# Kernel tuning notes

Measured on AMD Instinct MI355X. Metric: run time of the kernel, lower is better.

## Reference

```python
import jax, jax.numpy as jnp
import numpy as np

B, T, D, H, L, V = 16, 1024, 512, 8, 6, 96
HS = D // H
FF = 4 * D


def setup_inputs() -> dict:
    key = jax.random.key(0)
    ks = jax.random.split(key, 16)
    n = lambda k, shape: jax.random.normal(k, shape, jnp.float32) * 0.02
    return {
        "idx": jax.random.randint(ks[0], (B, T), 0, V),
        "targets": jax.random.randint(ks[1], (B, T), 0, V),
        "tok_emb": n(ks[2], (V, D)),
        "pos_emb": n(ks[3], (T, D)),
        "Wq": n(ks[4], (L, H, D, HS)),
        "Wk": n(ks[5], (L, H, D, HS)),
        "Wv": n(ks[6], (L, H, D, HS)),
        "Wproj": n(ks[7], (L, D, D)),
        "bproj": jnp.zeros((L, D), jnp.float32),
        "W1": n(ks[8], (L, D, FF)),
        "b1": jnp.zeros((L, FF), jnp.float32),
        "W2": n(ks[9], (L, FF, D)),
        "b2": jnp.zeros((L, D), jnp.float32),
        "ln1_s": jnp.ones((L, D), jnp.float32),
        "ln1_b": jnp.zeros((L, D), jnp.float32),
        "ln2_s": jnp.ones((L, D), jnp.float32),
        "ln2_b": jnp.zeros((L, D), jnp.float32),
        "lnf_s": jnp.ones((D,), jnp.float32),
        "lnf_b": jnp.zeros((D,), jnp.float32),
        "Wout": n(ks[10], (D, V)),
        "bout": jnp.zeros((V,), jnp.float32),
    }


def _ln(x, s, b, eps=1e-5):
    m = x.mean(-1, keepdims=True)
    v = ((x - m) ** 2).mean(-1, keepdims=True)
    return (x - m) * jax.lax.rsqrt(v + eps) * s + b


def reference(idx, targets, tok_emb, pos_emb, Wq, Wk, Wv, Wproj, bproj,
              W1, b1, W2, b2, ln1_s, ln1_b, ln2_s, ln2_b, lnf_s, lnf_b,
              Wout, bout):
    x = tok_emb[idx] + pos_emb[:T]  # [B,T,D]
    causal = jnp.tril(jnp.ones((T, T), jnp.bool_))
    scale = D ** (-0.5)  # NOTE: source scales by full channel dim, not head_size
    for l in range(L):
        h = _ln(x, ln1_s[l], ln1_b[l])
        q = jnp.einsum("btd,hdk->bhtk", h, Wq[l])
        k = jnp.einsum("btd,hdk->bhtk", h, Wk[l])
        v = jnp.einsum("btd,hdk->bhtk", h, Wv[l])
        att = jnp.einsum("bhtk,bhsk->bhts", q, k) * scale
        att = jnp.where(causal, att, -jnp.inf)
        att = jax.nn.softmax(att, axis=-1)
        o = jnp.einsum("bhts,bhsk->bhtk", att, v)
        o = o.transpose(0, 2, 1, 3).reshape(B, T, D)  # concat heads
        x = x + (o @ Wproj[l] + bproj[l])
        h2 = _ln(x, ln2_s[l], ln2_b[l])
        x = x + (jnp.maximum(h2 @ W1[l] + b1[l], 0.0) @ W2[l] + b2[l])
    x = _ln(x, lnf_s, lnf_b)
    logits = (x @ Wout + bout).reshape(B * T, V)
    logp = jax.nn.log_softmax(logits, axis=-1)
    loss = -logp[jnp.arange(B * T), targets.reshape(-1)].mean()
    return logits, loss
```

## Files before the change

kernel.cpp:

```cpp
#include <hip/hip_runtime.h>

#define B_  16
#define T_  1024
#define D_  512
#define H_  8
#define L_  6
#define V_  96
#define HS_ 64
#define FF_ 2048
#define BT_ (B_*T_)
#define QKS 1024

typedef __attribute__((ext_vector_type(8))) short bf16x8;
typedef __attribute__((ext_vector_type(4))) float f32x4;

typedef __attribute__((address_space(3))) unsigned int lds_u32_t;
typedef const __attribute__((address_space(1))) unsigned int glb_u32_t;

__device__ __forceinline__ void gload16(const unsigned short* g, unsigned short* l) {
  __builtin_amdgcn_global_load_lds((glb_u32_t*)g, (lds_u32_t*)l, 16, 0, 0);
}

__device__ __forceinline__ unsigned short f2b(float f) {
  unsigned u = __float_as_uint(f);
  unsigned r = (u + 0x7FFFu + ((u >> 16) & 1u)) >> 16;
  return (unsigned short)r;
}

__global__ void zero_kernel(float* p) { p[0] = 0.f; }

__global__ __launch_bounds__(128) void embed_kernel(const int* __restrict__ idx,
    const float* __restrict__ tok, const float* __restrict__ pos, float* __restrict__ x) {
  int bt = blockIdx.x;
  int t  = bt & (T_ - 1);
  int id = idx[bt];
  if (id < 0) id = 0; if (id > V_ - 1) id = V_ - 1;
  int d  = threadIdx.x * 4;
  float4 tv = *(const float4*)(tok + (size_t)id * D_ + d);
  float4 pv = *(const float4*)(pos + (size_t)t  * D_ + d);
  float4 o = {tv.x + pv.x, tv.y + pv.y, tv.z + pv.z, tv.w + pv.w};
  *(float4*)(x + (size_t)bt * D_ + d) = o;
}

__global__ __launch_bounds__(256) void transpose_cvt(const float* __restrict__ src,
    unsigned short* __restrict__ dst, int R, int C, long sstride, long dstride,
    int zper, long zouter) {
  __shared__ float t[32][33];
  const float* s = src + (size_t)blockIdx.z * sstride;
  unsigned short* d = dst + (size_t)(blockIdx.z / zper) * zouter
                          + (size_t)(blockIdx.z % zper) * dstride;
  int r0 = blockIdx.y * 32, c0 = blockIdx.x * 32;
  int tr = threadIdx.x >> 5, tc = threadIdx.x & 31;
#pragma unroll
  for (int i = 0; i < 4; ++i)
    t[tr + i * 8][tc] = s[(size_t)(r0 + tr + i * 8) * C + c0 + tc];
  __syncthreads();
#pragma unroll
  for (int i = 0; i < 4; ++i)
    d[(size_t)(c0 + tr + i * 8) * R + r0 + tc] = f2b(t[tc][tr + i * 8]);
}

template<bool BF16OUT>
__global__ __launch_bounds__(256) void ln_kernel(const float* __restrict__ x,
    const float* __restrict__ s, const float* __restrict__ b, void* __restrict__ outv) {
  int wave = threadIdx.x >> 6;
  int lane = threadIdx.x & 63;
  int r = blockIdx.x * 4 + wave;
  const float* xr = x + (size_t)r * D_ + lane * 8;
  float4 va = *(const float4*)(xr);
  float4 vb = *(const float4*)(xr + 4);
  float vals[8] = {va.x, va.y, va.z, va.w, vb.x, vb.y, vb.z, vb.w};
  float sum = 0.f;
#pragma unroll
  for (int j = 0; j < 8; ++j) sum += vals[j];
#pragma unroll
  for (int o = 32; o > 0; o >>= 1) sum += __shfl_xor(sum, o, 64);
  float mean = sum * (1.f / D_);
  float vs = 0.f;
#pragma unroll
  for (int j = 0; j < 8; ++j) { float d = vals[j] - mean; vs += d * d; }
#pragma unroll
  for (int o = 32; o > 0; o >>= 1) vs += __shfl_xor(vs, o, 64);
  float rstd = rsqrtf(vs * (1.f / D_) + 1e-5f);
  float4 sa = *(const float4*)(s + lane * 8);
  float4 sb = *(const float4*)(s + lane * 8 + 4);
  float4 ba = *(const float4*)(b + lane * 8);
  float4 bb = *(const float4*)(b + lane * 8 + 4);
  float sc[8] = {sa.x, sa.y, sa.z, sa.w, sb.x, sb.y, sb.z, sb.w};
  float bc[8] = {ba.x, ba.y, ba.z, ba.w, bb.x, bb.y, bb.z, bb.w};
  float v[8];
#pragma unroll
  for (int j = 0; j < 8; ++j) v[j] = (vals[j] - mean) * rstd * sc[j] + bc[j];
  if (BF16OUT) {
    uint4 pk;
    pk.x = (unsigned)f2b(v[0]) | ((unsigned)f2b(v[1]) << 16);
    pk.y = (unsigned)f2b(v[2]) | ((unsigned)f2b(v[3]) << 16);
    pk.z = (unsigned)f2b(v[4]) | ((unsigned)f2b(v[5]) << 16);
    pk.w = (unsigned)f2b(v[6]) | ((unsigned)f2b(v[7]) << 16);
    *(uint4*)((unsigned short*)outv + (size_t)r * D_ + lane * 8) = pk;
  } else {
    float* op = (float*)outv + (size_t)r * D_ + lane * 8;
    *(float4*)(op)     = make_float4(v[0], v[1], v[2], v[3]);
    *(float4*)(op + 4) = make_float4(v[4], v[5], v[6], v[7]);
  }
}

#define BK 32
template<bool ACC, bool RELU, bool BIAS, int OUTMODE, int MT, int NT>
__global__ __launch_bounds__(256) void mfma_gemm(
    const unsigned short* __restrict__ A,
    const unsigned short* __restrict__ Bt,
    const float* __restrict__ bias,
    void* __restrict__ Cv, void* __restrict__ Cv2,
    int K, int ldc) {
  constexpr int NI = (MT == 128) ? 4 : (NT == 128 ? 2 : 1);
  constexpr int WN = (MT == 128) ? 64 : (NT == 128 ? 32 : 16);
  __shared__ unsigned short Al[2][MT * BK];
  __shared__ unsigned short Bl[2][NT * BK];
  const int nwg = gridDim.x * gridDim.y;
  const int flat = blockIdx.x + gridDim.x * blockIdx.y;
  const int swz = (flat & 7) * (nwg >> 3) + (flat >> 3);
  const int bx = swz / gridDim.y;
  const int by = swz % gridDim.y;
  const int m0 = bx * MT, n0 = by * NT;
  const int tid = threadIdx.x;
  const int lane = tid & 63, wave = tid >> 6;
  const int wy = (MT == 128) ? (wave >> 1) : 0;
  const int wx = (MT == 128) ? (wave & 1) : wave;
  const int l15 = lane & 15, quad = lane >> 4;

  const int sbase = wave * 1024;
  const int soff  = sbase + lane * 16;
  const int r0 = soff >> 6, c0e = (soff & 63) >> 1;
  const int r1 = r0 + 64;
  const int ls = sbase >> 1;
  const unsigned short* gA0 = A  + (size_t)(m0 + r0) * K + c0e;
  const unsigned short* gA1 = A  + (size_t)(m0 + r1) * K + c0e;
  const unsigned short* gB0 = Bt + (size_t)(n0 + r0) * K + c0e;
  const unsigned short* gB1 = Bt + (size_t)(n0 + r1) * K + c0e;

  auto stage = [&](int buf, int k0) {
    gload16(gA0 + k0, &Al[buf][ls]);
    if constexpr (MT == 128) gload16(gA1 + k0, &Al[buf][ls + 2048]);
    gload16(gB0 + k0, &Bl[buf][ls]);
    if constexpr (NT == 128) gload16(gB1 + k0, &Bl[buf][ls + 2048]);
  };

  f32x4 acc[4][NI];
  const f32x4 z4 = {0.f, 0.f, 0.f, 0.f};
#pragma unroll
  for (int mi = 0; mi < 4; ++mi)
#pragma unroll
    for (int ni = 0; ni < NI; ++ni) acc[mi][ni] = z4;

  stage(0, 0);
  __syncthreads();

  const int nsteps = K / BK;
  int cur = 0;
  for (int s = 0; s < nsteps; ++s) {
    if (s + 1 < nsteps) stage(cur ^ 1, (s + 1) * BK);
    bf16x8 af[4], bfr[NI];
#pragma unroll
    for (int mi = 0; mi < 4; ++mi)
      af[mi] = *(const bf16x8*)(&Al[cur][(wy * 64 + mi * 16 + l15) * BK + quad * 8]);
#pragma unroll
    for (int ni = 0; ni < NI; ++ni)
      bfr[ni] = *(const bf16x8*)(&Bl[cur][(wx * WN + ni * 16 + l15) * BK + quad * 8]);
#pragma unroll
    for (int mi = 0; mi < 4; ++mi)
#pragma unroll
      for (int ni = 0; ni < NI; ++ni)
        acc[mi][ni] = __builtin_amdgcn_mfma_f32_16x16x32_bf16(af[mi], bfr[ni], acc[mi][ni], 0, 0, 0);
    if (s + 1 < nsteps) {
      __syncthreads();
      cur ^= 1;
    }
  }

#pragma unroll
  for (int mi = 0; mi < 4; ++mi) {
    int row0 = m0 + wy * 64 + mi * 16 + quad * 4;
#pragma unroll
    for (int ni = 0; ni < NI; ++ni) {
      int col = n0 + wx * WN + ni * 16 + l15;
      float bb = BIAS ? bias[col] : 0.f;
#pragma unroll
      for (int r = 0; r < 4; ++r) {
        float v = acc[mi][ni][r] + bb;
        if (RELU) v = fmaxf(v, 0.f);
        int row = row0 + r;
        if (OUTMODE == 3) {
          if (col < 1024) {
            ((unsigned short*)Cv)[(size_t)row * QKS + col] = f2b(v);
          } else {
            int vcol = col - 1024;
            int b = row >> 10, t = row & (T_ - 1);
            int h = vcol >> 6, hs = vcol & 63;
            ((unsigned short*)Cv2)[((size_t)((b * H_ + h) * HS_ + hs)) * T_ + t] = f2b(v);
          }
        } else {
          size_t off = (size_t)row * ldc + col;
          if (ACC) v += ((const float*)Cv)[off];
          if (OUTMODE == 1) ((unsigned short*)Cv)[off] = f2b(v);
          else              ((float*)Cv)[off] = v;
        }
      }
    }
  }
}

#define PSTR 72
__global__ __launch_bounds__(256) void attn_mfma(const unsigned short* __restrict__ q,
    const unsigned short* __restrict__ k, const unsigned short* __restrict__ vt,
    unsigned short* __restrict__ o) {
  __shared__ unsigned short Pbuf[2][64 * PSTR];
  __shared__ float Lsum[4][64];
  const int bh = blockIdx.y;
  const int b = bh >> 3, hh = bh & 7;
  const int tid = threadIdx.x;
  const int lane = tid & 63, w = tid >> 6;
  const int l15 = lane & 15, quad = lane >> 4;
  const float CEXP = 0.044194173824159216f * 1.4426950408889634f;

  const unsigned short* kbase = k  + (size_t)(b * T_ + w * 16 + l15) * QKS + hh * HS_ + quad * 8;
  const unsigned short* vbase = vt + ((size_t)(bh * HS_ + w * 16 + l15)) * T_ + quad * 8;
  const int gc = w * 16 + l15;
  const f32x4 z4 = {0.f, 0.f, 0.f, 0.f};

  for (int pass = 0; pass < 2; ++pass) {
    const int qt = pass ? (int)blockIdx.x : (T_ / 64 - 1 - (int)blockIdx.x);

    bf16x8 qf[4][2];
#pragma unroll
    for (int mi = 0; mi < 4; ++mi)
#pragma unroll
      for (int c = 0; c < 2; ++c)
        qf[mi][c] = *(const bf16x8*)(q + (size_t)(b * T_ + qt * 64 + mi * 16 + l15) * QKS
                                       + hh * HS_ + c * 32 + quad * 8);

    f32x4 oacc[4];
    float psum[4][4];
#pragma unroll
    for (int mi = 0; mi < 4; ++mi) {
      oacc[mi] = z4;
#pragma unroll
      for (int r = 0; r < 4; ++r) psum[mi][r] = 0.f;
    }

    bf16x8 kf[2], vf[2];
#pragma unroll
    for (int c = 0; c < 2; ++c) {
      kf[c] = *(const bf16x8*)(kbase + c * 32);
      vf[c] = *(const bf16x8*)(vbase + c * 32);
    }

    for (int kt = 0; kt <= qt; ++kt) {
      const int ktn = (kt < qt) ? kt + 1 : qt;
      bf16x8 kfn[2], vfn[2];
#pragma unroll
      for (int c = 0; c < 2; ++c) {
        kfn[c] = *(const bf16x8*)(kbase + (size_t)ktn * 64 * QKS + c * 32);
        vfn[c] = *(const bf16x8*)(vbase + ktn * 64 + c * 32);
      }

      f32x4 s[4];
#pragma unroll
      for (int mi = 0; mi < 4; ++mi) s[mi] = z4;
      __builtin_amdgcn_s_setprio(1);
#pragma unroll
      for (int c = 0; c < 2; ++c)
#pragma unroll
        for (int mi = 0; mi < 4; ++mi)
          s[mi] = __builtin_amdgcn_mfma_f32_16x16x32_bf16(qf[mi][c], kf[c], s[mi], 0, 0, 0);
      __builtin_amdgcn_s_setprio(0);

      unsigned short* pb = Pbuf[kt & 1];
      const bool diag = (kt == qt);
#pragma unroll
      for (int mi = 0; mi < 4; ++mi) {
        const int row0 = mi * 16 + quad * 4;
        float pv_[4];
#pragma unroll
        for (int r = 0; r < 4; ++r) {
          float p = exp2f(s[mi][r] * CEXP);
          if (diag && gc > row0 + r) p = 0.f;
          psum[mi][r] += p;
          pv_[r] = p;
        }
        unsigned pk01, pk23;
        asm("v_cvt_pk_bf16_f32 %0, %1, %2" : "=v"(pk01) : "v"(pv_[0]), "v"(pv_[1]));
        asm("v_cvt_pk_bf16_f32 %0, %1, %2" : "=v"(pk23) : "v"(pv_[2]), "v"(pv_[3]));
        const int base = row0 * PSTR + gc;
        pb[base]            = (unsigned short)(pk01 & 0xFFFFu);
        pb[base + PSTR]     = (unsigned short)(pk01 >> 16);
        pb[base + 2 * PSTR] = (unsigned short)(pk23 & 0xFFFFu);
        pb[base + 3 * PSTR] = (unsigned short)(pk23 >> 16);
      }
      __syncthreads();
      __builtin_amdgcn_s_setprio(1);
#pragma unroll
      for (int c = 0; c < 2; ++c) {
#pragma unroll
        for (int mi = 0; mi < 4; ++mi) {
          bf16x8 pf = *(const bf16x8*)(&pb[(mi * 16 + l15) * PSTR + c * 32 + quad * 8]);
          oacc[mi] = __builtin_amdgcn_mfma_f32_16x16x32_bf16(pf, vf[c], oacc[mi], 0, 0, 0);
        }
      }
      __builtin_amdgcn_s_setprio(0);
#pragma unroll
      for (int c = 0; c < 2; ++c) { kf[c] = kfn[c]; vf[c] = vfn[c]; }
    }

#pragma unroll
    for (int mi = 0; mi < 4; ++mi)
#pragma unroll
      for (int r = 0; r < 4; ++r) {
#pragma unroll
        for (int off = 1; off < 16; off <<= 1)
          psum[mi][r] += __shfl_xor(psum[mi][r], off, 64);
      }
    if (l15 == 0) {
#pragma unroll
      for (int mi = 0; mi < 4; ++mi)
#pragma unroll
        for (int r = 0; r < 4; ++r)
          Lsum[w][mi * 16 + quad * 4 + r] = psum[mi][r];
    }
    __syncthreads();
#pragma unroll
    for (int mi = 0; mi < 4; ++mi)
#pragma unroll
      for (int r = 0; r < 4; ++r) {
        int row = mi * 16 + quad * 4 + r;
        float inv = 1.f / (Lsum[0][row] + Lsum[1][row] + Lsum[2][row] + Lsum[3][row]);
        o[(size_t)(b * T_ + qt * 64 + row) * D_ + hh * HS_ + w * 16 + l15] =
            f2b(oacc[mi][r] * inv);
      }
  }
}

__global__ __launch_bounds__(256) void gemm_f32_kernel(const float* __restrict__ A, int lda,
    const float* __restrict__ Bw, int ldb, const float* __restrict__ bias,
    float* __restrict__ C, int ldc, int K, int N) {
  __shared__ float As[16][64];
  __shared__ float Bs[16][64];
  int n0 = blockIdx.y * 64;
  int nv = N - n0; if (nv > 64) nv = 64;
  int m0 = blockIdx.x * 64;
  const int tid = threadIdx.x;
  const int tx = tid & 15, ty = tid >> 4;
  const int amm = tid >> 2;
  const int akk = (tid & 3) * 4;
  const int bkk = tid >> 4;
  const int bnn = (tid & 15) * 4;
  float acc[4][4] = {};
  for (int k0 = 0; k0 < K; k0 += 16) {
    float4 av = *(const float4*)(A + (size_t)(m0 + amm) * lda + k0 + akk);
    As[akk + 0][amm] = av.x; As[akk + 1][amm] = av.y;
    As[akk + 2][amm] = av.z; As[akk + 3][amm] = av.w;
    if (bnn < nv) {
      float4 bv = *(const float4*)(Bw + (size_t)(k0 + bkk) * ldb + n0 + bnn);
      Bs[bkk][bnn + 0] = bv.x; Bs[bkk][bnn + 1] = bv.y;
      Bs[bkk][bnn + 2] = bv.z; Bs[bkk][bnn + 3] = bv.w;
    } else {
      Bs[bkk][bnn + 0] = 0.f; Bs[bkk][bnn + 1] = 0.f;
      Bs[bkk][bnn + 2] = 0.f; Bs[bkk][bnn + 3] = 0.f;
    }
    __syncthreads();
#pragma unroll
    for (int kk = 0; kk < 16; ++kk) {
      float4 a4 = *(const float4*)(&As[kk][ty * 4]);
      float4 b4 = *(const float4*)(&Bs[kk][tx * 4]);
      float aa[4] = {a4.x, a4.y, a4.z, a4.w};
      float bb[4] = {b4.x, b4.y, b4.z, b4.w};
#pragma unroll
      for (int i = 0; i < 4; ++i)
#pragma unroll
        for (int j = 0; j < 4; ++j)
          acc[i][j] = fmaf(aa[i], bb[j], acc[i][j]);
    }
    __syncthreads();
  }
  if (tx * 4 < nv) {
#pragma unroll
    for (int i = 0; i < 4; ++i) {
      float* cp = C + (size_t)(m0 + ty * 4 + i) * ldc + n0 + tx * 4;
      float4 st = {acc[i][0] + bias[n0 + tx * 4 + 0], acc[i][1] + bias[n0 + tx * 4 + 1],
                   acc[i][2] + bias[n0 + tx * 4 + 2], acc[i][3] + bias[n0 + tx * 4 + 3]};
      *(float4*)cp = st;
    }
  }
}

__global__ __launch_bounds__(256) void loss_kernel(const float* __restrict__ logits,
    const int* __restrict__ targets, float* __restrict__ loss_acc) {
  __shared__ float wsum[4];
  int wave = threadIdx.x >> 6, lane = threadIdx.x & 63;
  float local = 0.f;
  for (int r = blockIdx.x * 4 + wave; r < BT_; r += gridDim.x * 4) {
    const float* lr = logits + (size_t)r * V_;
    float v0 = lr[lane];
    float v1 = (lane < 32) ? lr[64 + lane] : -INFINITY;
    float mx = fmaxf(v0, v1);
#pragma unroll
    for (int o = 32; o > 0; o >>= 1) mx = fmaxf(mx, __shfl_xor(mx, o, 64));
    float se = expf(v0 - mx) + ((lane < 32) ? expf(v1 - mx) : 0.f);
#pragma unroll
    for (int o = 32; o > 0; o >>= 1) se += __shfl_xor(se, o, 64);
    if (lane == 0) {
      int tg = targets[r];
      if (tg < 0) tg = 0; if (tg > V_ - 1) tg = V_ - 1;
      local += (mx + logf(se)) - lr[tg];
    }
  }
  if (lane == 0) wsum[wave] = local;
  __syncthreads();
  if (threadIdx.x == 0)
    atomicAdd(loss_acc, wsum[0] + wsum[1] + wsum[2] + wsum[3]);
}

__global__ void loss_finalize_kernel(const float* __restrict__ acc, float* __restrict__ out) {
  out[(size_t)BT_ * V_] = acc[0] * (1.f / BT_);
}

static void* g_ws_fallback = nullptr;

extern "C" void kernel_launch(void* const* d_in, const int* in_sizes, int n_in,
                              void* d_out, int out_size, void* d_ws, size_t ws_size,
                              hipStream_t stream) {
  const int*   idx     = (const int*)d_in[0];
  const int*   targets = (const int*)d_in[1];
  const float* tok  = (const float*)d_in[2];
  const float* pos  = (const float*)d_in[3];
  const float* Wq   = (const float*)d_in[4];
  const float* Wk   = (const float*)d_in[5];
  const float* Wv   = (const float*)d_in[6];
  const float* Wp   = (const float*)d_in[7];
  const float* bp   = (const float*)d_in[8];
  const float* W1   = (const float*)d_in[9];
  const float* b1   = (const float*)d_in[10];
  const float* W2   = (const float*)d_in[11];
  const float* b2   = (const float*)d_in[12];
  const float* l1s  = (const float*)d_in[13];
  const float* l1b  = (const float*)d_in[14];
  const float* l2s  = (const float*)d_in[15];
  const float* l2b  = (const float*)d_in[16];
  const float* lfs  = (const float*)d_in[17];
  const float* lfb  = (const float*)d_in[18];
  const float* Wout = (const float*)d_in[19];
  const float* bout = (const float*)d_in[20];
  float* out = (float*)d_out;

  const size_t n_x  = (size_t)BT_ * D_;
  const size_t n_wT = 9437184;
  const size_t need_floats = n_x + n_x + n_x / 2 + n_x / 2 + n_x / 2 +
                             (size_t)BT_ * FF_ / 2 + n_wT + 256;
  const size_t need_bytes  = need_floats * sizeof(float);

  float* ws;
  if (ws_size >= need_bytes) {
    ws = (float*)d_ws;
  } else {
    if (!g_ws_fallback) (void)hipMalloc(&g_ws_fallback, need_bytes);
    ws = (float*)g_ws_fallback;
  }

  size_t off = 0;
  float* x  = ws + off; off += n_x;
  float* qf32 = ws + off; off += n_x;
  unsigned short* qkb = (unsigned short*)qf32;
  unsigned short* spare = (unsigned short*)(ws + off); off += n_x / 2;
  unsigned short* vtb = (unsigned short*)(ws + off); off += n_x / 2;
  unsigned short* hb  = (unsigned short*)(ws + off); off += n_x / 2;
  unsigned short* ffb = (unsigned short*)(ws + off); off += (size_t)BT_ * FF_ / 2;
  unsigned short* wqkvT = (unsigned short*)(ws + off);
  unsigned short* wpT = wqkvT + (size_t)L_ * 3 * D_ * D_;
  unsigned short* w1T = wpT + (size_t)L_ * D_ * D_;
  unsigned short* w2T = w1T + (size_t)L_ * D_ * FF_;
  off += n_wT;
  float* lacc = ws + off;
  (void)spare;

  const long DD = (long)D_ * D_;
  const long L3DD = 3 * DD;

  zero_kernel<<<1, 1, 0, stream>>>(lacc);
  embed_kernel<<<BT_, 128, 0, stream>>>(idx, tok, pos, x);

  transpose_cvt<<<dim3(2, 16, 48), 256, 0, stream>>>(Wq, wqkvT,            512, 64, 32768, 32768, 8, L3DD);
  transpose_cvt<<<dim3(2, 16, 48), 256, 0, stream>>>(Wk, wqkvT + DD,       512, 64, 32768, 32768, 8, L3DD);
  transpose_cvt<<<dim3(2, 16, 48), 256, 0, stream>>>(Wv, wqkvT + 2 * DD,   512, 64, 32768, 32768, 8, L3DD);
  transpose_cvt<<<dim3(16, 16, 6), 256, 0, stream>>>(Wp, wpT, 512, 512, 262144, 0, 1, 262144);
  transpose_cvt<<<dim3(64, 16, 6), 256, 0, stream>>>(W1, w1T, 512, 2048, 1048576, 0, 1, 1048576);
  transpose_cvt<<<dim3(16, 64, 6), 256, 0, stream>>>(W2, w2T, 2048, 512, 1048576, 0, 1, 1048576);

  const dim3 gQKV(BT_ / 128, 12);
  const dim3 gF(BT_ / 128, FF_ / 128);
  const dim3 gD64(BT_ / 64, D_ / 128);

  for (int l = 0; l < L_; ++l) {
    ln_kernel<true><<<BT_ / 4, 256, 0, stream>>>(x, l1s + (size_t)l * D_, l1b + (size_t)l * D_, hb);
    mfma_gemm<false, false, false, 3, 128, 128><<<gQKV, 256, 0, stream>>>(
        hb, wqkvT + (size_t)l * L3DD, nullptr, qkb, vtb, D_, 0);
    attn_mfma<<<dim3(T_ / 128, B_ * H_), 256, 0, stream>>>(qkb, qkb + 512, vtb, hb);
    mfma_gemm<true, false, true, 0, 64, 128><<<gD64, 256, 0, stream>>>(
        hb, wpT + (size_t)l * DD, bp + (size_t)l * D_, x, nullptr, D_, D_);
    ln_kernel<true><<<BT_ / 4, 256, 0, stream>>>(x, l2s + (size_t)l * D_, l2b + (size_t)l * D_, hb);
    mfma_gemm<false, true, true, 1, 128, 128><<<gF, 256, 0, stream>>>(
        hb, w1T + (size_t)l * D_ * FF_, b1 + (size_t)l * FF_, ffb, nullptr, D_, FF_);
    mfma_gemm<true, false, true, 0, 64, 128><<<gD64, 256, 0, stream>>>(
        ffb, w2T + (size_t)l * FF_ * D_, b2 + (size_t)l * D_, x, nullptr, FF_, D_);
  }

  ln_kernel<false><<<BT_ / 4, 256, 0, stream>>>(x, lfs, lfb, qf32);
  gemm_f32_kernel<<<dim3(BT_ / 64, 2), 256, 0, stream>>>(
      qf32, D_, Wout, V_, bout, out, V_, D_, V_);
  loss_kernel<<<1024, 256, 0, stream>>>(out, targets, lacc);
  loss_finalize_kernel<<<1, 1, 0, stream>>>(lacc, out);
}
```

Measured before the change: 1.832 ms.

## Split K across two wave groups in residual-accumulate GEMMs with LDS reduction

Adds a WG2 mode to the MFMA GEMM. It launches 512 threads as two 4-wave groups, and each group computes half of the K dimension into its own double-buffered LDS tiles. Group 1 writes its partial accumulators to a shared LDS buffer, and group 0 adds them before the epilogue. It is applied to the projection and FFN-down GEMMs (64x128 tiles, f32 accumulate) to give each workgroup more waves and latency hiding. The cost is more LDS per block (an extra 32KB reduction buffer plus duplicated tiles) and a reduction step, which may lower occupancy.

```diff
diff --git a/kernel.cpp b/kernel.cpp
--- a/kernel.cpp
+++ b/kernel.cpp
@@ -106,17 +106,20 @@
 }
 
 #define BK 32
-template<bool ACC, bool RELU, bool BIAS, int OUTMODE, int MT, int NT>
-__global__ __launch_bounds__(256) void mfma_gemm(
+template<bool ACC, bool RELU, bool BIAS, int OUTMODE, int MT, int NT, bool WG2>
+__global__ __launch_bounds__(WG2 ? 512 : 256) void mfma_gemm(
     const unsigned short* __restrict__ A,
     const unsigned short* __restrict__ Bt,
     const float* __restrict__ bias,
     void* __restrict__ Cv, void* __restrict__ Cv2,
     int K, int ldc) {
+  static_assert(!WG2 || (OUTMODE == 0 && ACC && !RELU), "WG2 path is f32-ACC only");
   constexpr int NI = (MT == 128) ? 4 : (NT == 128 ? 2 : 1);
   constexpr int WN = (MT == 128) ? 64 : (NT == 128 ? 32 : 16);
-  __shared__ unsigned short Al[2][MT * BK];
-  __shared__ unsigned short Bl[2][NT * BK];
+  constexpr int NG = WG2 ? 2 : 1;
+  __shared__ unsigned short Al[NG][2][MT * BK];
+  __shared__ unsigned short Bl[NG][2][NT * BK];
+  __shared__ float red[WG2 ? (MT * NT) : 4];
   const int nwg = gridDim.x * gridDim.y;
   const int flat = blockIdx.x + gridDim.x * blockIdx.y;
   const int swz = (flat & 7) * (nwg >> 3) + (flat >> 3);
@@ -125,25 +128,28 @@
   const int m0 = bx * MT, n0 = by * NT;
   const int tid = threadIdx.x;
   const int lane = tid & 63, wave = tid >> 6;
-  const int wy = (MT == 128) ? (wave >> 1) : 0;
-  const int wx = (MT == 128) ? (wave & 1) : wave;
+  const int grp = WG2 ? (wave >> 2) : 0;
+  const int wl  = WG2 ? (wave & 3) : wave;
+  const int wy = (MT == 128) ? (wl >> 1) : 0;
+  const int wx = (MT == 128) ? (wl & 1) : wl;
   const int l15 = lane & 15, quad = lane >> 4;
 
-  const int sbase = wave * 1024;
+  const int sbase = wl * 1024;
   const int soff  = sbase + lane * 16;
   const int r0 = soff >> 6, c0e = (soff & 63) >> 1;
   const int r1 = r0 + 64;
   const int ls = sbase >> 1;
-  const unsigned short* gA0 = A  + (size_t)(m0 + r0) * K + c0e;
-  const unsigned short* gA1 = A  + (size_t)(m0 + r1) * K + c0e;
-  const unsigned short* gB0 = Bt + (size_t)(n0 + r0) * K + c0e;
-  const unsigned short* gB1 = Bt + (size_t)(n0 + r1) * K + c0e;
+  const int kb = grp * (K / NG);
+  const unsigned short* gA0 = A  + (size_t)(m0 + r0) * K + c0e + kb;
+  const unsigned short* gA1 = A  + (size_t)(m0 + r1) * K + c0e + kb;
+  const unsigned short* gB0 = Bt + (size_t)(n0 + r0) * K + c0e + kb;
+  const unsigned short* gB1 = Bt + (size_t)(n0 + r1) * K + c0e + kb;
 
   auto stage = [&](int buf, int k0) {
-    gload16(gA0 + k0, &Al[buf][ls]);
-    if constexpr (MT == 128) gload16(gA1 + k0, &Al[buf][ls + 2048]);
-    gload16(gB0 + k0, &Bl[buf][ls]);
-    if constexpr (NT == 128) gload16(gB1 + k0, &Bl[buf][ls + 2048]);
+    gload16(gA0 + k0, &Al[grp][buf][ls]);
+    if constexpr (MT == 128) gload16(gA1 + k0, &Al[grp][buf][ls + 2048]);
+    gload16(gB0 + k0, &Bl[grp][buf][ls]);
+    if constexpr (NT == 128) gload16(gB1 + k0, &Bl[grp][buf][ls + 2048]);
   };
 
   f32x4 acc[4][NI];
@@ -156,17 +162,17 @@
   stage(0, 0);
   __syncthreads();
 
-  const int nsteps = K / BK;
+  const int nsteps = K / NG / BK;
   int cur = 0;
   for (int s = 0; s < nsteps; ++s) {
     if (s + 1 < nsteps) stage(cur ^ 1, (s + 1) * BK);
     bf16x8 af[4], bfr[NI];
 #pragma unroll
     for (int mi = 0; mi < 4; ++mi)
-      af[mi] = *(const bf16x8*)(&Al[cur][(wy * 64 + mi * 16 + l15) * BK + quad * 8]);
+      af[mi] = *(const bf16x8*)(&Al[grp][cur][(wy * 64 + mi * 16 + l15) * BK + quad * 8]);
 #pragma unroll
     for (int ni = 0; ni < NI; ++ni)
-      bfr[ni] = *(const bf16x8*)(&Bl[cur][(wx * WN + ni * 16 + l15) * BK + quad * 8]);
+      bfr[ni] = *(const bf16x8*)(&Bl[grp][cur][(wx * WN + ni * 16 + l15) * BK + quad * 8]);
 #pragma unroll
     for (int mi = 0; mi < 4; ++mi)
 #pragma unroll
@@ -176,6 +182,27 @@
       __syncthreads();
       cur ^= 1;
     }
+  }
+
+  if constexpr (WG2) {
+    if (grp == 1) {
+#pragma unroll
+      for (int mi = 0; mi < 4; ++mi)
+#pragma unroll
+        for (int ni = 0; ni < NI; ++ni)
+#pragma unroll
+          for (int r = 0; r < 4; ++r)
+            red[((mi * NI + ni) * 4 + r) * 256 + wl * 64 + lane] = acc[mi][ni][r];
+    }
+    __syncthreads();
+    if (grp == 1) return;
+#pragma unroll
+    for (int mi = 0; mi < 4; ++mi)
+#pragma unroll
+      for (int ni = 0; ni < NI; ++ni)
+#pragma unroll
+        for (int r = 0; r < 4; ++r)
+          acc[mi][ni][r] += red[((mi * NI + ni) * 4 + r) * 256 + wl * 64 + lane];
   }
 
 #pragma unroll
@@ -501,15 +528,15 @@
 
   for (int l = 0; l < L_; ++l) {
     ln_kernel<true><<<BT_ / 4, 256, 0, stream>>>(x, l1s + (size_t)l * D_, l1b + (size_t)l * D_, hb);
-    mfma_gemm<false, false, false, 3, 128, 128><<<gQKV, 256, 0, stream>>>(
+    mfma_gemm<false, false, false, 3, 128, 128, false><<<gQKV, 256, 0, stream>>>(
         hb, wqkvT + (size_t)l * L3DD, nullptr, qkb, vtb, D_, 0);
     attn_mfma<<<dim3(T_ / 128, B_ * H_), 256, 0, stream>>>(qkb, qkb + 512, vtb, hb);
-    mfma_gemm<true, false, true, 0, 64, 128><<<gD64, 256, 0, stream>>>(
+    mfma_gemm<true, false, true, 0, 64, 128, true><<<gD64, 512, 0, stream>>>(
         hb, wpT + (size_t)l * DD, bp + (size_t)l * D_, x, nullptr, D_, D_);
     ln_kernel<true><<<BT_ / 4, 256, 0, stream>>>(x, l2s + (size_t)l * D_, l2b + (size_t)l * D_, hb);
-    mfma_gemm<false, true, true, 1, 128, 128><<<gF, 256, 0, stream>>>(
+    mfma_gemm<false, true, true, 1, 128, 128, false><<<gF, 256, 0, stream>>>(
         hb, w1T + (size_t)l * D_ * FF_, b1 + (size_t)l * FF_, ffb, nullptr, D_, FF_);
-    mfma_gemm<true, false, true, 0, 64, 128><<<gD64, 256, 0, stream>>>(
+    mfma_gemm<true, false, true, 0, 64, 128, true><<<gD64, 512, 0, stream>>>(
         ffb, w2T + (size_t)l * FF_ * D_, b2 + (size_t)l * D_, x, nullptr, FF_, D_);
   }
 
```

After: 1.986 ms. 8.4% more time.
